# Performance work log

Hardware: AMD Instinct MI355X
Metric: run time of the kernel (lower is better)

The kernel has to match this reference:

```python
import jax, jax.numpy as jnp
import numpy as np

B, S, H_SZ = 1, 2048, 2048
E, K, KVH, D = 8, 2, 16, 128      # experts, top_k, kv heads, head_dim
QH = K * KVH                       # 32 query heads
QSZ = KVH * D                      # 2048 per-expert q/o size


def setup_inputs() -> dict:
    key = jax.random.key(0)
    ks = jax.random.split(key, 6)
    hidden_states = jax.random.normal(ks[0], (B, S, H_SZ), jnp.float32)
    causal = jnp.tril(jnp.ones((S, S), dtype=bool))
    attention_bias = jnp.where(causal, 0.0, -1e9).astype(jnp.float32)[None, None]  # [1,1,S,S]
    inv_freq = 1.0 / (10000.0 ** (jnp.arange(0, D, 2, dtype=jnp.float32) / D))     # [D/2]
    ang = jnp.arange(S, dtype=jnp.float32)[:, None] * inv_freq[None, :]            # [S,D/2]
    cos, sin = jnp.cos(ang), jnp.sin(ang)
    router_w = jax.random.normal(ks[1], (E, H_SZ), jnp.float32) * 0.02
    q_w = jax.random.normal(ks[2], (E, QSZ, H_SZ), jnp.float32) * 0.02
    o_w = jax.random.normal(ks[3], (E, H_SZ, QSZ), jnp.float32) * 0.02
    kv_w = jax.random.normal(ks[4], (2 * QSZ, H_SZ), jnp.float32) * 0.02
    bias = jax.random.normal(ks[5], (H_SZ,), jnp.float32) * 0.02
    return {"hidden_states": hidden_states, "attention_bias": attention_bias,
            "cos": cos, "sin": sin, "router_w": router_w, "q_w": q_w,
            "o_w": o_w, "kv_w": kv_w, "bias": bias}


def _rope(x, cos, sin):
    # x: [b,s,h,d]; half-rotation rotary, cos/sin: [s,d/2]
    d2 = x.shape[-1] // 2
    x1, x2 = x[..., :d2], x[..., d2:]
    c = cos[None, :, None, :]
    s = sin[None, :, None, :]
    return jnp.concatenate([x1 * c - x2 * s, x1 * s + x2 * c], axis=-1)


def reference(hidden_states, attention_bias, cos, sin, router_w, q_w, o_w, kv_w, bias):
    # ---- router: top-k + softmax over top-k logits ----
    logits = jnp.einsum('bsh,eh->bse', hidden_states, router_w)         # [b,s,E]
    top_vals, sel = jax.lax.top_k(logits, K)                            # [b,s,K]
    gates = jax.nn.softmax(top_vals, axis=-1)                           # [b,s,K]
    # ---- per-expert Q projections (dense, as in original), gather selected ----
    q_all = jnp.einsum('bsh,eqh->bseq', hidden_states, q_w)             # [b,s,E,QSZ]
    q_sel = jnp.take_along_axis(q_all, sel[..., None], axis=2)          # [b,s,K,QSZ]
    # slots -> kv-major head layout: [b,s,K,KVH,D] -> [b,s,KVH,K,D] -> [b,s,QH,D]
    q = q_sel.reshape(B, S, K, KVH, D).transpose(0, 1, 3, 2, 4).reshape(B, S, QH, D)
    # ---- shared K/V ----
    kv = jnp.einsum('bsh,oh->bso', hidden_states, kv_w)                 # [b,s,2*QSZ]
    k_st, v_st = jnp.split(kv, 2, axis=-1)
    k_st = k_st.reshape(B, S, KVH, D)
    v_st = v_st.reshape(B, S, KVH, D)
    # ---- rotary ----
    q = _rope(q, cos, sin)
    k_st = _rope(k_st, cos, sin)
    # ---- GQA attention (group size K; kv-major query layout matches repeat) ----
    k_rep = jnp.repeat(k_st, K, axis=2)                                 # [b,s,QH,D]
    v_rep = jnp.repeat(v_st, K, axis=2)
    scale = D ** -0.5
    scores = jnp.einsum('bqhd,bkhd->bhqk', q, k_rep) * scale + attention_bias
    probs = jax.nn.softmax(scores, axis=-1)
    attn = jnp.einsum('bhqk,bkhd->bqhd', probs, v_rep)                  # [b,s,QH,D]
    # back to slot-major: [b,s,KVH,K,D] -> [b,s,K,KVH,D] -> [b,s,K,QSZ]
    attn4 = attn.reshape(B, S, KVH, K, D).transpose(0, 1, 3, 2, 4).reshape(B, S, K, QSZ)
    # ---- per-expert O projections, masked + gated sum (as in original) ----
    out = jnp.zeros((B, S, H_SZ), hidden_states.dtype)
    for e in range(E):
        o_e = jnp.einsum('bskq,hq->bskh', attn4, o_w[e])                # [b,s,K,H]
        m = (sel == e).astype(hidden_states.dtype) * gates              # [b,s,K]
        out = out + jnp.einsum('bsk,bskh->bsh', m, o_e)
    return out + bias
```

## Files before the change

### kernel.cpp

```cpp
#include <hip/hip_runtime.h>
#include <hip/hip_bf16.h>
#include <stdint.h>

#define S_LEN 2048
#define HSZ 2048
#define NE 8
#define TOPK 2
#define NKVH 16
#define HD 128
#define NQH 32
#define QSZ 2048

typedef __attribute__((ext_vector_type(8))) __bf16 bf16x8;
typedef __attribute__((ext_vector_type(4))) float f32x4;

#define BM 128
#define BN 128
#define BK 64

__device__ __forceinline__ void gload_lds16(const void* g, void* l) {
  __builtin_amdgcn_global_load_lds((__attribute__((address_space(1))) void*)g,
                                   (__attribute__((address_space(3))) void*)l, 16, 0, 0);
}

__device__ __forceinline__ bf16x8 pack8(float4 a, float4 b) {
  bf16x8 r;
  r[0] = (__bf16)a.x; r[1] = (__bf16)a.y; r[2] = (__bf16)a.z; r[3] = (__bf16)a.w;
  r[4] = (__bf16)b.x; r[5] = (__bf16)b.y; r[6] = (__bf16)b.z; r[7] = (__bf16)b.w;
  return r;
}

__global__ __launch_bounds__(256) void cast_kernel(const float* __restrict__ src,
                                                   __bf16* __restrict__ dst, long n) {
  long i0 = ((long)blockIdx.x * 256 + threadIdx.x) * 4;
  long stride = (long)gridDim.x * 256 * 4;
  for (long i = i0; i < n; i += stride) {
    float4 v = *(const float4*)(src + i);
    unsigned short a = __builtin_bit_cast(unsigned short, (__bf16)v.x);
    unsigned short b = __builtin_bit_cast(unsigned short, (__bf16)v.y);
    unsigned short c = __builtin_bit_cast(unsigned short, (__bf16)v.z);
    unsigned short d = __builtin_bit_cast(unsigned short, (__bf16)v.w);
    uint2 o;
    o.x = (unsigned)a | ((unsigned)b << 16);
    o.y = (unsigned)c | ((unsigned)d << 16);
    *(uint2*)(dst + i) = o;
  }
}

__global__ __launch_bounds__(256) void router_kernel(const float* __restrict__ hs,
                                                     const float* __restrict__ rw,
                                                     int* __restrict__ sel,
                                                     float* __restrict__ gates) {
  const int s = blockIdx.x * 4 + (threadIdx.x >> 6);
  const int lane = threadIdx.x & 63;
  const float* row = hs + (size_t)s * HSZ;
  float acc[NE];
#pragma unroll
  for (int e = 0; e < NE; ++e) acc[e] = 0.f;
  for (int j = lane; j < HSZ; j += 64) {
    float x = row[j];
#pragma unroll
    for (int e = 0; e < NE; ++e) acc[e] += x * rw[e * HSZ + j];
  }
#pragma unroll
  for (int e = 0; e < NE; ++e) {
#pragma unroll
    for (int off = 32; off > 0; off >>= 1) acc[e] += __shfl_xor(acc[e], off);
  }
  if (lane == 0) {
    int i0 = 0; float v0 = acc[0];
#pragma unroll
    for (int e = 1; e < NE; ++e) if (acc[e] > v0) { v0 = acc[e]; i0 = e; }
    int i1 = -1; float v1 = -1e30f;
#pragma unroll
    for (int e = 0; e < NE; ++e) if (e != i0 && acc[e] > v1) { v1 = acc[e]; i1 = e; }
    float ge = __expf(v1 - v0);
    float den = 1.f + ge;
    sel[s * 2] = i0; sel[s * 2 + 1] = i1;
    gates[s * 2] = 1.f / den; gates[s * 2 + 1] = ge / den;
  }
}

__global__ void bucket_kernel(const int* __restrict__ sel, int* __restrict__ pair_list,
                              int* __restrict__ expert_off) {
  __shared__ int cnt[NE], base[NE];
  const int t = threadIdx.x;
  if (t < NE) cnt[t] = 0;
  __syncthreads();
  for (int p2 = t; p2 < S_LEN * TOPK; p2 += 256) atomicAdd(&cnt[sel[p2]], 1);
  __syncthreads();
  if (t == 0) {
    int run = 0;
#pragma unroll
    for (int e = 0; e < NE; ++e) { base[e] = run; expert_off[e] = run; run += cnt[e]; }
    expert_off[NE] = run;
  }
  __syncthreads();
  for (int p2 = t; p2 < S_LEN * TOPK; p2 += 256) {
    int pos = atomicAdd(&base[sel[p2]], 1);
    pair_list[pos] = p2;
  }
}

template <int MODE>
__global__ __launch_bounds__(256) void gemm_kernel(const __bf16* __restrict__ A_src,
                                                   const float* __restrict__ B_src,
                                                   const int* __restrict__ pair_list,
                                                   const int* __restrict__ expert_off,
                                                   const float* __restrict__ gates,
                                                   __bf16* __restrict__ out_bf,
                                                   __bf16* __restrict__ out_vT,
                                                   float* __restrict__ out_f32) {
  constexpr int KD = 2048;
  const int n0 = blockIdx.x * BN;
  const int m0 = blockIdx.y * BM;
  const int e = blockIdx.z;
  int start = 0, cntv = S_LEN;
  if constexpr (MODE != 0) {
    start = expert_off[e];
    cntv = expert_off[e + 1] - start;
    if (m0 >= cntv) return;
  }
  const float* Bb = B_src + (size_t)e * QSZ * HSZ;
  __shared__ __attribute__((aligned(16))) __bf16 As[BM * BK];
  __shared__ __attribute__((aligned(16))) __bf16 Bs[BN * BK];
  __shared__ const __bf16* a_rows[BM];
  __shared__ int row_pair[BM];
  const int t = threadIdx.x;
  if (t < BM) {
    if constexpr (MODE == 0) {
      a_rows[t] = A_src + (size_t)(m0 + t) * KD;
      row_pair[t] = 0;
    } else {
      int idx = m0 + t;
      bool valid = idx < cntv;
      int pp = pair_list[start + (valid ? idx : 0)];
      row_pair[t] = valid ? pp : -1;
      size_t arow = (MODE == 1) ? (size_t)(pp >> 1) : (size_t)pp;
      a_rows[t] = A_src + arow * (size_t)KD;
    }
  }
  __syncthreads();

  const int lane = t & 63, w = t >> 6;
  const int wr = (w >> 1) * 64, wc = (w & 1) * 64;
  const int lr = lane & 15, lk = (lane >> 4) * 8;
  const int sr = t >> 3;
  const int scol = (t & 7) * 8;

  const __bf16* arows_t[4];
#pragma unroll
  for (int it = 0; it < 4; ++it) arows_t[it] = a_rows[sr + it * 32];

  const int brow = t >> 2;
  const int bcol = (t & 3) * 16;
  const float* bptr0 = Bb + (size_t)(n0 + brow) * KD + bcol;
  const float* bptr1 = bptr0 + (size_t)64 * KD;
  __bf16* bs0 = Bs + brow * BK + bcol;
  __bf16* bs1 = Bs + (brow + 64) * BK + bcol;

  f32x4 acc[4][4];
#pragma unroll
  for (int m = 0; m < 4; ++m)
#pragma unroll
    for (int n = 0; n < 4; ++n) acc[m][n] = (f32x4)0.f;

  for (int k0 = 0; k0 < KD; k0 += BK) {
#pragma unroll
    for (int it = 0; it < 4; ++it)
      gload_lds16(arows_t[it] + k0 + scol, As + (sr + it * 32) * BK + scol);
    {
      float4 f0 = *(const float4*)(bptr0 + k0);
      float4 f1 = *(const float4*)(bptr0 + k0 + 4);
      float4 f2 = *(const float4*)(bptr0 + k0 + 8);
      float4 f3 = *(const float4*)(bptr0 + k0 + 12);
      float4 g0 = *(const float4*)(bptr1 + k0);
      float4 g1 = *(const float4*)(bptr1 + k0 + 4);
      float4 g2 = *(const float4*)(bptr1 + k0 + 8);
      float4 g3 = *(const float4*)(bptr1 + k0 + 12);
      *(bf16x8*)(bs0) = pack8(f0, f1);
      *(bf16x8*)(bs0 + 8) = pack8(f2, f3);
      *(bf16x8*)(bs1) = pack8(g0, g1);
      *(bf16x8*)(bs1 + 8) = pack8(g2, g3);
    }
    __syncthreads();
#pragma unroll
    for (int kk = 0; kk < BK; kk += 32) {
      bf16x8 af[4], bfv[4];
#pragma unroll
      for (int m = 0; m < 4; ++m) af[m] = *(const bf16x8*)(As + (size_t)(wr + m * 16 + lr) * BK + kk + lk);
#pragma unroll
      for (int n = 0; n < 4; ++n) bfv[n] = *(const bf16x8*)(Bs + (size_t)(wc + n * 16 + lr) * BK + kk + lk);
#pragma unroll
      for (int m = 0; m < 4; ++m)
#pragma unroll
        for (int n = 0; n < 4; ++n)
          acc[m][n] = __builtin_amdgcn_mfma_f32_16x16x32_bf16(af[m], bfv[n], acc[m][n], 0, 0, 0);
    }
    __syncthreads();
  }

  const int lg = lane >> 4;
  if constexpr (MODE == 0) {
    if (n0 < 2048) {
#pragma unroll
      for (int m = 0; m < 4; ++m)
#pragma unroll
        for (int r = 0; r < 4; ++r) {
          const int row = wr + m * 16 + lg * 4 + r;
#pragma unroll
          for (int n = 0; n < 4; ++n) {
            const int col = n0 + wc + n * 16 + lr;
            out_bf[(size_t)(m0 + row) * 2048 + col] = (__bf16)acc[m][n][r];
          }
        }
    } else {
#pragma unroll
      for (int m = 0; m < 4; ++m) {
        const int sb = m0 + wr + m * 16 + lg * 4;
#pragma unroll
        for (int n = 0; n < 4; ++n) {
          const int cv = n0 + wc + n * 16 + lr - 2048;
          uint2 pk;
          unsigned short h0 = __builtin_bit_cast(unsigned short, (__bf16)acc[m][n][0]);
          unsigned short h1 = __builtin_bit_cast(unsigned short, (__bf16)acc[m][n][1]);
          unsigned short h2 = __builtin_bit_cast(unsigned short, (__bf16)acc[m][n][2]);
          unsigned short h3 = __builtin_bit_cast(unsigned short, (__bf16)acc[m][n][3]);
          pk.x = (unsigned)h0 | ((unsigned)h1 << 16);
          pk.y = (unsigned)h2 | ((unsigned)h3 << 16);
          *(uint2*)(out_vT + (size_t)cv * S_LEN + sb) = pk;
        }
      }
    }
  } else {
#pragma unroll
    for (int m = 0; m < 4; ++m) {
#pragma unroll
      for (int r = 0; r < 4; ++r) {
        const int row = wr + m * 16 + lg * 4 + r;
        const int pp = row_pair[row];
        if (pp < 0) continue;
        if constexpr (MODE == 1) {
#pragma unroll
          for (int n = 0; n < 4; ++n) {
            const int col = n0 + wc + n * 16 + lr;
            out_bf[(size_t)pp * QSZ + col] = (__bf16)acc[m][n][r];
          }
        } else {
          const float gt = gates[pp];
#pragma unroll
          for (int n = 0; n < 4; ++n) {
            const int col = n0 + wc + n * 16 + lr;
            out_f32[(size_t)pp * HSZ + col] = acc[m][n][r] * gt;
          }
        }
      }
    }
  }
}

__global__ __launch_bounds__(256) void rope_q_kernel(const __bf16* __restrict__ q_lin,
                                                     const float* __restrict__ cosb,
                                                     const float* __restrict__ sinb,
                                                     __bf16* __restrict__ q_attn) {
  const int idx = blockIdx.x * 4 + (threadIdx.x >> 6);
  const int lane = threadIdx.x & 63;
  const int s = idx >> 5;
  const int h = idx & 31;
  const int kvh = h >> 1, k = h & 1;
  const __bf16* src = q_lin + ((size_t)s * 2 + k) * QSZ + kvh * HD;
  float x1 = (float)src[lane];
  float x2 = (float)src[lane + 64];
  float c = cosb[s * 64 + lane], sn = sinb[s * 64 + lane];
  __bf16* dst = q_attn + ((size_t)h * S_LEN + s) * HD;
  dst[lane] = (__bf16)(x1 * c - x2 * sn);
  dst[lane + 64] = (__bf16)(x1 * sn + x2 * c);
}

__global__ __launch_bounds__(256) void rope_k_kernel(const __bf16* __restrict__ kv_lin,
                                                     const float* __restrict__ cosb,
                                                     const float* __restrict__ sinb,
                                                     __bf16* __restrict__ k_attn) {
  const int idx = blockIdx.x * 4 + (threadIdx.x >> 6);
  const int lane = threadIdx.x & 63;
  const int s = idx >> 4;
  const int gq = idx & 15;
  const __bf16* ksrc = kv_lin + (size_t)s * 2048 + gq * HD;
  float x1 = (float)ksrc[lane], x2 = (float)ksrc[lane + 64];
  float c = cosb[s * 64 + lane], sn = sinb[s * 64 + lane];
  __bf16* kd = k_attn + ((size_t)gq * S_LEN + s) * HD;
  kd[lane] = (__bf16)(x1 * c - x2 * sn);
  kd[lane + 64] = (__bf16)(x1 * sn + x2 * c);
}

__global__ __launch_bounds__(256, 2) void attn_kernel(const __bf16* __restrict__ q_attn,
                                                      const __bf16* __restrict__ k_attn,
                                                      const __bf16* __restrict__ vT,
                                                      __bf16* __restrict__ attn4) {
  __shared__ __attribute__((aligned(16))) __bf16 Ks[2][64 * 128];
  __shared__ __attribute__((aligned(16))) __bf16 Vs[2][128 * 64];
  const int h = blockIdx.x;
  const int by = (blockIdx.y < 8) ? blockIdx.y : 23 - blockIdx.y;
  const int s0 = by * 128;
  const int t = threadIdx.x;
  const int lane = t & 63;
  const int w = t >> 6;
  const int g = lane >> 4;
  const int lr = lane & 15;
  const int kvh = h >> 1;

  int koff[4], voff[4];
#pragma unroll
  for (int i = 0; i < 4; ++i) {
    const int c = t + i * 256;
    const int kvL = c >> 4, w16 = c & 15;
    koff[i] = kvL * HD + ((w16 ^ (kvL & 7)) * 8);
    const int d = c >> 3, w8 = c & 7;
    voff[i] = d * S_LEN + ((w8 ^ (d & 7)) * 8);
  }
  const __bf16* Kb = k_attn + (size_t)kvh * S_LEN * HD;
  const __bf16* Vb = vT + (size_t)kvh * HD * S_LEN;

  auto stage = [&](int buf, int kv0) {
#pragma unroll
    for (int i = 0; i < 4; ++i) {
      const int c = t + i * 256;
      gload_lds16(Kb + (size_t)kv0 * HD + koff[i], (char*)Ks[buf] + c * 16);
      gload_lds16(Vb + (size_t)kv0 + voff[i], (char*)Vs[buf] + c * 16);
    }
  };

  bf16x8 qf[2][4];
#pragma unroll
  for (int m = 0; m < 2; ++m) {
    const __bf16* qbase = q_attn + ((size_t)h * S_LEN + s0 + w * 32 + m * 16 + lr) * HD;
#pragma unroll
    for (int ds = 0; ds < 4; ++ds) qf[m][ds] = *(const bf16x8*)(qbase + ds * 32 + g * 8);
  }

  float m_run[2] = {-1e30f, -1e30f}, l_run[2] = {0.f, 0.f};
  f32x4 acc[2][8];
#pragma unroll
  for (int m = 0; m < 2; ++m)
#pragma unroll
    for (int dt = 0; dt < 8; ++dt) acc[m][dt] = (f32x4)0.f;

  const int xr = (lr & 7) << 4;
  const int nt = 2 * by + 2;
  stage(0, 0);
  for (int ti = 0; ti < nt; ++ti) {
    const int cur = ti & 1;
    const int kv0 = ti * 64;
    __syncthreads();
    if (ti + 1 < nt) stage(cur ^ 1, kv0 + 64);

    f32x4 sc[2][4];
#pragma unroll
    for (int m = 0; m < 2; ++m)
#pragma unroll
      for (int b = 0; b < 4; ++b) sc[m][b] = (f32x4)0.f;
#pragma unroll
    for (int b = 0; b < 4; ++b) {
#pragma unroll
      for (int ds = 0; ds < 4; ++ds) {
        const bf16x8 kf = *(const bf16x8*)((const char*)Ks[cur] +
            (b * 16 + lr) * 256 + ((ds * 64 + g * 16) ^ xr));
        sc[0][b] = __builtin_amdgcn_mfma_f32_16x16x32_bf16(kf, qf[0][ds], sc[0][b], 0, 0, 0);
        sc[1][b] = __builtin_amdgcn_mfma_f32_16x16x32_bf16(kf, qf[1][ds], sc[1][b], 0, 0, 0);
      }
    }

    bf16x8 paf[2][2];
#pragma unroll
    for (int m = 0; m < 2; ++m) {
      const int qrow = s0 + w * 32 + m * 16 + lr;
      float p[4][4];
      float tmax = -1e30f;
#pragma unroll
      for (int b = 0; b < 4; ++b)
#pragma unroll
        for (int r = 0; r < 4; ++r) {
          const int kv = kv0 + b * 16 + g * 4 + r;
          float v = sc[m][b][r] * 0.08838834764831845f;
          if (kv > qrow) v = -1e30f;
          p[b][r] = v;
          tmax = fmaxf(tmax, v);
        }
      tmax = fmaxf(tmax, __shfl_xor(tmax, 16));
      tmax = fmaxf(tmax, __shfl_xor(tmax, 32));
      const float m_new = fmaxf(m_run[m], tmax);
      const float alpha = __expf(m_run[m] - m_new);
      float lsum = 0.f;
#pragma unroll
      for (int b = 0; b < 4; ++b)
#pragma unroll
        for (int r = 0; r < 4; ++r) {
          p[b][r] = __expf(p[b][r] - m_new);
          lsum += p[b][r];
        }
      lsum += __shfl_xor(lsum, 16);
      lsum += __shfl_xor(lsum, 32);
      l_run[m] = l_run[m] * alpha + lsum;
      m_run[m] = m_new;

      float ar[4];
#pragma unroll
      for (int r = 0; r < 4; ++r) ar[r] = __shfl(alpha, g * 4 + r);
#pragma unroll
      for (int dt = 0; dt < 8; ++dt)
#pragma unroll
        for (int r = 0; r < 4; ++r) acc[m][dt][r] *= ar[r];

#pragma unroll
      for (int half = 0; half < 2; ++half) {
        bf16x8 af;
#pragma unroll
        for (int j = 0; j < 8; ++j) {
          const int srcl = lr + 16 * ((g & 1) * 2 + (j >> 2));
          const float va = __shfl(p[half * 2][j & 3], srcl);
          const float vb = __shfl(p[half * 2 + 1][j & 3], srcl);
          af[j] = (__bf16)((g >> 1) ? vb : va);
        }
        paf[m][half] = af;
      }
    }

#pragma unroll
    for (int dt = 0; dt < 8; ++dt) {
      const char* vrow = (const char*)Vs[cur] + (dt * 16 + lr) * 128;
      const bf16x8 v0 = *(const bf16x8*)(vrow + ((g * 16) ^ xr));
      const bf16x8 v1 = *(const bf16x8*)(vrow + ((64 + g * 16) ^ xr));
      acc[0][dt] = __builtin_amdgcn_mfma_f32_16x16x32_bf16(paf[0][0], v0, acc[0][dt], 0, 0, 0);
      acc[0][dt] = __builtin_amdgcn_mfma_f32_16x16x32_bf16(paf[0][1], v1, acc[0][dt], 0, 0, 0);
      acc[1][dt] = __builtin_amdgcn_mfma_f32_16x16x32_bf16(paf[1][0], v0, acc[1][dt], 0, 0, 0);
      acc[1][dt] = __builtin_amdgcn_mfma_f32_16x16x32_bf16(paf[1][1], v1, acc[1][dt], 0, 0, 0);
    }
  }

#pragma unroll
  for (int m = 0; m < 2; ++m) {
    const float li = 1.f / l_run[m];
    float linv[4];
#pragma unroll
    for (int r = 0; r < 4; ++r) linv[r] = __shfl(li, g * 4 + r);
#pragma unroll
    for (int dt = 0; dt < 8; ++dt)
#pragma unroll
      for (int r = 0; r < 4; ++r) {
        const int qg = s0 + w * 32 + m * 16 + g * 4 + r;
        attn4[((size_t)qg * 2 + (h & 1)) * QSZ + kvh * HD + dt * 16 + lr] =
            (__bf16)(acc[m][dt][r] * linv[r]);
      }
  }
}

__global__ __launch_bounds__(256) void final_kernel(const float* __restrict__ o_tmp,
                                                    const float* __restrict__ bias,
                                                    float* __restrict__ out) {
  const size_t i = ((size_t)blockIdx.x * 256 + threadIdx.x) * 4;
  const int s = (int)(i >> 11);
  const int hcol = (int)(i & 2047);
  float4 a = *(const float4*)(o_tmp + ((size_t)s * 2) * HSZ + hcol);
  float4 b = *(const float4*)(o_tmp + ((size_t)s * 2 + 1) * HSZ + hcol);
  float4 bb = *(const float4*)(bias + hcol);
  float4 o;
  o.x = a.x + b.x + bb.x; o.y = a.y + b.y + bb.y;
  o.z = a.z + b.z + bb.z; o.w = a.w + b.w + bb.w;
  *(float4*)(out + i) = o;
}

extern "C" void kernel_launch(void* const* d_in, const int* in_sizes, int n_in,
                              void* d_out, int out_size, void* d_ws, size_t ws_size,
                              hipStream_t stream) {
  (void)in_sizes; (void)n_in; (void)out_size; (void)ws_size;
  const float* hs = (const float*)d_in[0];
  const float* cosb = (const float*)d_in[2];
  const float* sinb = (const float*)d_in[3];
  const float* rw = (const float*)d_in[4];
  const float* qw = (const float*)d_in[5];
  const float* ow = (const float*)d_in[6];
  const float* kvw = (const float*)d_in[7];
  const float* bias = (const float*)d_in[8];
  float* outp = (float*)d_out;

  char* base = (char*)d_ws;
  size_t off = 0;
  auto take = [&](size_t bytes) {
    char* r = base + off;
    off += (bytes + 255) & ~(size_t)255;
    return r;
  };
  __bf16* hid_bf  = (__bf16*)take((size_t)S_LEN * HSZ * 2);
  __bf16* k_attn  = (__bf16*)take((size_t)NKVH * S_LEN * HD * 2);
  __bf16* v_attnT = (__bf16*)take((size_t)NKVH * HD * S_LEN * 2);
  char* bufA = take((size_t)S_LEN * 4096 * 2);
  char* bufBC = take((size_t)S_LEN * TOPK * HSZ * 4);
  int* sel = (int*)take((size_t)S_LEN * TOPK * 4);
  float* gates = (float*)take((size_t)S_LEN * TOPK * 4);
  int* pair_list = (int*)take((size_t)S_LEN * TOPK * 4);
  int* expert_off = (int*)take((size_t)(NE + 1) * 4);

  __bf16* kv_lin = (__bf16*)bufA;
  __bf16* attn4 = (__bf16*)bufA;
  __bf16* q_lin = (__bf16*)bufBC;
  __bf16* q_attn = (__bf16*)(bufBC + (size_t)16 * 1024 * 1024);
  float* o_tmp = (float*)bufBC;

  cast_kernel<<<1024, 256, 0, stream>>>(hs, hid_bf, (long)S_LEN * HSZ);
  router_kernel<<<S_LEN / 4, 256, 0, stream>>>(hs, rw, sel, gates);
  bucket_kernel<<<1, 256, 0, stream>>>(sel, pair_list, expert_off);
  gemm_kernel<0><<<dim3(4096 / BN, S_LEN / BM, 1), 256, 0, stream>>>(
      hid_bf, kvw, nullptr, nullptr, nullptr, kv_lin, v_attnT, nullptr);
  rope_k_kernel<<<S_LEN * NKVH / 4, 256, 0, stream>>>(kv_lin, cosb, sinb, k_attn);
  gemm_kernel<1><<<dim3(QSZ / BN, 32, NE), 256, 0, stream>>>(
      hid_bf, qw, pair_list, expert_off, nullptr, q_lin, nullptr, nullptr);
  rope_q_kernel<<<S_LEN * NQH / 4, 256, 0, stream>>>(q_lin, cosb, sinb, q_attn);
  attn_kernel<<<dim3(NQH, 16), 256, 0, stream>>>(q_attn, k_attn, v_attnT, attn4);
  gemm_kernel<2><<<dim3(HSZ / BN, 32, NE), 256, 0, stream>>>(
      attn4, ow, pair_list, expert_off, gates, nullptr, nullptr, o_tmp);
  final_kernel<<<(S_LEN * HSZ / 4) / 256, 256, 0, stream>>>(o_tmp, bias, outp);
}
```

Before: 440.8 us.

## Double-buffer GEMM LDS tiles with register prefetch and XOR-swizzled layout

Splits the A and B shared-memory tiles into two buffers, so the global loads for the next K-tile are issued before the MFMA work on the current one. This leaves one barrier per iteration instead of two. The B tile is prefetched into registers and converted to bf16 at the top of the next iteration. An XOR swizzle on the 16-byte column chunks is applied to both tiles to cut LDS bank conflicts on the fragment reads. The cost is twice the LDS footprint, which may lower occupancy, and correctness now depends on the async LDS loads finishing before the single barrier.

Result: faster. 428.8 us (-2.7%).

```diff
diff --git a/kernel.cpp b/kernel.cpp
--- a/kernel.cpp
+++ b/kernel.cpp
@@ -112,6 +112,7 @@
                                                    __bf16* __restrict__ out_vT,
                                                    float* __restrict__ out_f32) {
   constexpr int KD = 2048;
+  constexpr int NT = KD / BK;
   const int n0 = blockIdx.x * BN;
   const int m0 = blockIdx.y * BM;
   const int e = blockIdx.z;
@@ -122,8 +123,8 @@
     if (m0 >= cntv) return;
   }
   const float* Bb = B_src + (size_t)e * QSZ * HSZ;
-  __shared__ __attribute__((aligned(16))) __bf16 As[BM * BK];
-  __shared__ __attribute__((aligned(16))) __bf16 Bs[BN * BK];
+  __shared__ __attribute__((aligned(16))) __bf16 As[2][BM * BK];
+  __shared__ __attribute__((aligned(16))) __bf16 Bs[2][BN * BK];
   __shared__ const __bf16* a_rows[BM];
   __shared__ int row_pair[BM];
   const int t = threadIdx.x;
@@ -144,20 +145,27 @@
 
   const int lane = t & 63, w = t >> 6;
   const int wr = (w >> 1) * 64, wc = (w & 1) * 64;
-  const int lr = lane & 15, lk = (lane >> 4) * 8;
-  const int sr = t >> 3;
-  const int scol = (t & 7) * 8;
-
-  const __bf16* arows_t[4];
-#pragma unroll
-  for (int it = 0; it < 4; ++it) arows_t[it] = a_rows[sr + it * 32];
+  const int lr = lane & 15, g = lane >> 4;
+  const int xa = lr & 7;
+
+  const __bf16* a_srow[4];
+  int a_soff[4];
+#pragma unroll
+  for (int i = 0; i < 4; ++i) {
+    const int c = t + i * 256;
+    const int row = c >> 3, win = c & 7;
+    a_srow[i] = a_rows[row];
+    a_soff[i] = (win ^ (row & 7)) * 8;
+  }
 
   const int brow = t >> 2;
-  const int bcol = (t & 3) * 16;
-  const float* bptr0 = Bb + (size_t)(n0 + brow) * KD + bcol;
-  const float* bptr1 = bptr0 + (size_t)64 * KD;
-  __bf16* bs0 = Bs + brow * BK + bcol;
-  __bf16* bs1 = Bs + (brow + 64) * BK + bcol;
+  const int bq = t & 3;
+  const float* bp0 = Bb + (size_t)(n0 + brow) * KD + bq * 16;
+  const float* bp1 = bp0 + (size_t)64 * KD;
+  const int c0 = (2 * bq) ^ (brow & 7);
+  const int c1 = (2 * bq + 1) ^ (brow & 7);
+  const int bo00 = brow * BK + c0 * 8, bo01 = brow * BK + c1 * 8;
+  const int bo10 = (brow + 64) * BK + c0 * 8, bo11 = (brow + 64) * BK + c1 * 8;
 
   f32x4 acc[4][4];
 #pragma unroll
@@ -165,39 +173,51 @@
 #pragma unroll
     for (int n = 0; n < 4; ++n) acc[m][n] = (f32x4)0.f;
 
-  for (int k0 = 0; k0 < KD; k0 += BK) {
-#pragma unroll
-    for (int it = 0; it < 4; ++it)
-      gload_lds16(arows_t[it] + k0 + scol, As + (sr + it * 32) * BK + scol);
-    {
-      float4 f0 = *(const float4*)(bptr0 + k0);
-      float4 f1 = *(const float4*)(bptr0 + k0 + 4);
-      float4 f2 = *(const float4*)(bptr0 + k0 + 8);
-      float4 f3 = *(const float4*)(bptr0 + k0 + 12);
-      float4 g0 = *(const float4*)(bptr1 + k0);
-      float4 g1 = *(const float4*)(bptr1 + k0 + 4);
-      float4 g2 = *(const float4*)(bptr1 + k0 + 8);
-      float4 g3 = *(const float4*)(bptr1 + k0 + 12);
-      *(bf16x8*)(bs0) = pack8(f0, f1);
-      *(bf16x8*)(bs0 + 8) = pack8(f2, f3);
-      *(bf16x8*)(bs1) = pack8(g0, g1);
-      *(bf16x8*)(bs1 + 8) = pack8(g2, g3);
-    }
+#pragma unroll
+  for (int i = 0; i < 4; ++i)
+    gload_lds16(a_srow[i] + a_soff[i], (char*)As[0] + (t + i * 256) * 16);
+  float4 cA0 = *(const float4*)(bp0), cA1 = *(const float4*)(bp0 + 4);
+  float4 cA2 = *(const float4*)(bp0 + 8), cA3 = *(const float4*)(bp0 + 12);
+  float4 cB0 = *(const float4*)(bp1), cB1 = *(const float4*)(bp1 + 4);
+  float4 cB2 = *(const float4*)(bp1 + 8), cB3 = *(const float4*)(bp1 + 12);
+
+#pragma unroll 2
+  for (int ti = 0; ti < NT; ++ti) {
+    const int cur = ti & 1;
+    *(bf16x8*)(&Bs[cur][bo00]) = pack8(cA0, cA1);
+    *(bf16x8*)(&Bs[cur][bo01]) = pack8(cA2, cA3);
+    *(bf16x8*)(&Bs[cur][bo10]) = pack8(cB0, cB1);
+    *(bf16x8*)(&Bs[cur][bo11]) = pack8(cB2, cB3);
     __syncthreads();
+
+    if (ti + 1 < NT) {
+      const int k1 = (ti + 1) * BK;
+#pragma unroll
+      for (int i = 0; i < 4; ++i)
+        gload_lds16(a_srow[i] + k1 + a_soff[i], (char*)As[cur ^ 1] + (t + i * 256) * 16);
+      cA0 = *(const float4*)(bp0 + k1); cA1 = *(const float4*)(bp0 + k1 + 4);
+      cA2 = *(const float4*)(bp0 + k1 + 8); cA3 = *(const float4*)(bp0 + k1 + 12);
+      cB0 = *(const float4*)(bp1 + k1); cB1 = *(const float4*)(bp1 + k1 + 4);
+      cB2 = *(const float4*)(bp1 + k1 + 8); cB3 = *(const float4*)(bp1 + k1 + 12);
+    }
+    __builtin_amdgcn_sched_barrier(0);
+
 #pragma unroll
     for (int kk = 0; kk < BK; kk += 32) {
       bf16x8 af[4], bfv[4];
 #pragma unroll
-      for (int m = 0; m < 4; ++m) af[m] = *(const bf16x8*)(As + (size_t)(wr + m * 16 + lr) * BK + kk + lk);
-#pragma unroll
-      for (int n = 0; n < 4; ++n) bfv[n] = *(const bf16x8*)(Bs + (size_t)(wc + n * 16 + lr) * BK + kk + lk);
+      for (int m = 0; m < 4; ++m)
+        af[m] = *(const bf16x8*)(&As[cur][(wr + m * 16 + lr) * BK + (((kk >> 3) + g) ^ xa) * 8]);
+#pragma unroll
+      for (int n = 0; n < 4; ++n)
+        bfv[n] = *(const bf16x8*)(&Bs[cur][(wc + n * 16 + lr) * BK + (((kk >> 3) + g) ^ xa) * 8]);
 #pragma unroll
       for (int m = 0; m < 4; ++m)
 #pragma unroll
         for (int n = 0; n < 4; ++n)
           acc[m][n] = __builtin_amdgcn_mfma_f32_16x16x32_bf16(af[m], bfv[n], acc[m][n], 0, 0, 0);
     }
-    __syncthreads();
+    __builtin_amdgcn_sched_barrier(0);
   }
 
   const int lg = lane >> 4;
```
